# Kernel optimization log

Measured on AMD Instinct MI355X. Metric: run time of the kernel, lower is better.

Reference implementation:

```python
import jax, jax.numpy as jnp
import numpy as np

N = 50000   # nodes
E = 800000  # edges (avg degree 16)
D = 64      # node_feature_dim == node_embedding_dim
L = 4       # num_layers
G = 64      # number of graphs in the batch


def setup_inputs() -> dict:
    key = jax.random.key(0)
    ks = jax.random.split(key, 6)
    x = jax.random.normal(ks[0], (N, D), dtype=jnp.float32)
    edge_index = jax.random.randint(ks[1], (2, E), 0, N, dtype=jnp.int32)
    batch = jnp.sort(jax.random.randint(ks[2], (N,), 0, G, dtype=jnp.int32))
    scale = 1.0 / np.sqrt(D)
    conv_W = jax.random.normal(ks[3], (L, D, D), dtype=jnp.float32) * scale
    conv_b = jnp.zeros((L, D), dtype=jnp.float32)
    lin_W = jax.random.normal(ks[4], (D, 1), dtype=jnp.float32) * scale
    lin_b = jnp.zeros((1,), dtype=jnp.float32)
    return dict(x=x, conv_W=conv_W, conv_b=conv_b, lin_W=lin_W, lin_b=lin_b,
                edge_index=edge_index, batch=batch)


def reference(x, conv_W, conv_b, lin_W, lin_b, edge_index, batch):
    n = x.shape[0]
    # GCNConv: add self-loops, symmetric deg^{-1/2} normalization (computed once; graph is static)
    loop = jnp.arange(n, dtype=edge_index.dtype)
    src = jnp.concatenate([edge_index[0], loop])
    dst = jnp.concatenate([edge_index[1], loop])
    deg = jax.ops.segment_sum(jnp.ones_like(dst, dtype=x.dtype), dst, num_segments=n)
    dinv = jnp.where(deg > 0, jax.lax.rsqrt(deg), 0.0)
    norm = (dinv[src] * dinv[dst])[:, None]  # [E+N, 1]
    # stacked GCNConv + ReLU
    for l in range(conv_W.shape[0]):
        h = x @ conv_W[l]                                       # [N, D] linear transform
        agg = jax.ops.segment_sum(norm * h[src], dst, num_segments=n)  # gather-normalize-scatter
        x = jax.nn.relu(agg + conv_b[l])
    # global_mean_pool over graphs
    counts = jax.ops.segment_sum(jnp.ones((n,), x.dtype), batch, num_segments=G)
    sums = jax.ops.segment_sum(x, batch, num_segments=G)        # [G, D]
    pooled = sums / jnp.maximum(counts, 1.0)[:, None]
    return pooled @ lin_W + lin_b                               # [G, 1]
```

## Files before the change

### kernel.cpp

```cpp
#include <hip/hip_runtime.h>


#define D 64
#define BSHIFT 10
#define BNODES 1024
#define EPT 16
#define CB (256 * EPT)
#define CAP 24576
#define SW(r, c4) ((c4) ^ (((r) >> 2) & 15))


__global__ __launch_bounds__(256) void setup_kernel(
        const float* __restrict__ W, float* __restrict__ Wt,
        int* __restrict__ bcnt, int L) {
    int b = blockIdx.x;
    if (b < L) {
        const float* w = W + (size_t)b * D * D;
        float* wt = Wt + (size_t)b * D * D;
        for (int idx = threadIdx.x; idx < D * D; idx += 256) {
            int k = idx >> 6, c = idx & 63;
            wt[c * D + k] = w[idx];
        }
    } else {
        bcnt[threadIdx.x] = 0;
    }
}


__global__ __launch_bounds__(256) void partition_kernel(
        const int* __restrict__ src, const int* __restrict__ dst,
        int* __restrict__ bcnt, unsigned* __restrict__ eb, int e) {
    __shared__ int cB[256], gb[256], cur[256];
    int t = threadIdx.x;
    cB[t] = 0;
    __syncthreads();
    int base = blockIdx.x * CB;
    int ps[EPT], pd[EPT];
    #pragma unroll
    for (int k = 0; k < EPT; ++k) {
        int i = base + t + k * 256;
        if (i < e) {
            ps[k] = src[i];
            pd[k] = dst[i];
            atomicAdd(&cB[pd[k] >> BSHIFT], 1);
        } else {
            pd[k] = -1;
        }
    }
    __syncthreads();
    if (cB[t]) gb[t] = atomicAdd(&bcnt[t], cB[t]);
    cur[t] = 0;
    __syncthreads();
    #pragma unroll
    for (int k = 0; k < EPT; ++k) {
        if (pd[k] >= 0) {
            int b = pd[k] >> BSHIFT;
            int p = atomicAdd(&cur[b], 1);
            eb[(size_t)b * CAP + gb[b] + p] =
                (unsigned)(ps[k] & 0xFFFF) | ((unsigned)(pd[k] & (BNODES - 1)) << 16);
        }
    }
}

__global__ __launch_bounds__(256) void boff_kernel(
        const int* __restrict__ bcnt, int* __restrict__ boff,
        int* __restrict__ row_start, int n, int e, int nb) {
    __shared__ int sh[256];
    int t = threadIdx.x;
    int c = (t < nb) ? bcnt[t] : 0;
    sh[t] = c;
    __syncthreads();
    for (int off = 1; off < 256; off <<= 1) {
        int vp = (t >= off) ? sh[t - off] : 0;
        __syncthreads();
        sh[t] += vp;
        __syncthreads();
    }
    if (t < nb) boff[t] = sh[t] - c;
    if (t == 255) boff[nb] = sh[255];
    if (t == 0) row_start[n] = e;
}

__global__ __launch_bounds__(BNODES) void build_csr(
        const unsigned* __restrict__ eb, const int* __restrict__ bcnt,
        const int* __restrict__ boff, int* __restrict__ row_start,
        float* __restrict__ dinv, int* __restrict__ csr_src, int n) {
    __shared__ int sh[BNODES];
    __shared__ int cur[BNODES];
    int b = blockIdx.x, t = threadIdx.x;
    int cnt = bcnt[b];
    const unsigned* ebb = eb + (size_t)b * CAP;
    sh[t] = 0;
    __syncthreads();
    for (int i = t; i < cnt; i += BNODES) atomicAdd(&sh[ebb[i] >> 16], 1);
    __syncthreads();
    int c = sh[t];
    __syncthreads();
    for (int off = 1; off < BNODES; off <<= 1) {
        int vp = (t >= off) ? sh[t - off] : 0;
        __syncthreads();
        sh[t] += vp;
        __syncthreads();
    }
    int a = sh[t] - c + boff[b];
    int node = b * BNODES + t;
    if (node < n) {
        row_start[node] = a;
        dinv[node] = 1.0f / sqrtf((float)(c + 1));
    }
    cur[t] = a;
    __syncthreads();
    for (int i = t; i < cnt; i += BNODES) {
        unsigned v = ebb[i];
        int p = atomicAdd(&cur[v >> 16], 1);
        csr_src[p] = (int)(v & 0xFFFFu);
    }
}


__global__ __launch_bounds__(256, 3) void matmul_kernel(
        const float* __restrict__ X, const float* __restrict__ Wt,
        const float* __restrict__ dinv, float* __restrict__ H, int n) {
    __shared__ float4 Xs[64 * 16];
    __shared__ float4 Ws[64 * 16];
    int t = threadIdx.x;
    int rowBase = blockIdx.x * 64;
    const float4* X4 = (const float4*)X;
    const float4* Wt4 = (const float4*)Wt;
    #pragma unroll
    for (int p = 0; p < 4; ++p) {
        int rl = (t >> 4) + 16 * p;
        int c4 = t & 15;
        int r = rowBase + rl;
        float4 v = make_float4(0.f, 0.f, 0.f, 0.f);
        if (r < n) v = X4[(size_t)r * 16 + c4];
        Xs[rl * 16 + SW(rl, c4)] = v;
        Ws[rl * 16 + SW(rl, c4)] = Wt4[rl * 16 + c4];
    }
    __syncthreads();
    int wv = t >> 6, lane = t & 63;
    int rg = lane >> 2, cg = lane & 3;
    int r0 = rg * 4;
    int c0 = wv * 16 + cg * 4;
    float acc[4][4] = {};
    #pragma unroll 2
    for (int k4 = 0; k4 < 16; ++k4) {
        float4 xv[4], wvv[4];
        #pragma unroll
        for (int i = 0; i < 4; ++i) xv[i] = Xs[(r0 + i) * 16 + SW(r0 + i, k4)];
        #pragma unroll
        for (int j = 0; j < 4; ++j) wvv[j] = Ws[(c0 + j) * 16 + SW(c0 + j, k4)];
        #pragma unroll
        for (int i = 0; i < 4; ++i)
            #pragma unroll
            for (int j = 0; j < 4; ++j) {
                acc[i][j] += xv[i].x * wvv[j].x;
                acc[i][j] += xv[i].y * wvv[j].y;
                acc[i][j] += xv[i].z * wvv[j].z;
                acc[i][j] += xv[i].w * wvv[j].w;
            }
    }
    #pragma unroll
    for (int i = 0; i < 4; ++i) {
        int r = rowBase + r0 + i;
        if (r < n) {
            float dr = dinv[r];
            float4 o = make_float4(dr * acc[i][0], dr * acc[i][1],
                                   dr * acc[i][2], dr * acc[i][3]);
            *(float4*)&H[(size_t)r * D + c0] = o;
        }
    }
}


__global__ __launch_bounds__(256) void agg_fused(
        const float* __restrict__ H, const int* __restrict__ csr_src,
        const int* __restrict__ row_start, const float* __restrict__ dinv,
        const float* __restrict__ bias, const float* __restrict__ Wtn,
        float* __restrict__ out, int n) {
    __shared__ float4 Wsh4[D * 16];
    __shared__ float rowsh[4][D];
    int t = threadIdx.x;
    {
        const float4* Wt4 = (const float4*)Wtn;
        #pragma unroll
        for (int p = 0; p < 4; ++p) {
            int i = t + p * 256;
            int c = i >> 4, k4 = i & 15;
            Wsh4[(c << 4) | (k4 ^ (c & 15))] = Wt4[i];
        }
    }
    __syncthreads();
    int wave = t >> 6, lane = t & 63;
    int v = blockIdx.x * 4 + wave;
    bool active = v < n;
    float dv = 0.f, o = 0.f;
    if (active) {
        dv = dinv[v];
        float acc = H[(size_t)v * D + lane];
        int s = row_start[v];
        int e = row_start[v + 1];
        int i = s;
        #pragma unroll 1
        for (; i + 16 <= e; i += 16) {
            int u[16];
            float h[16];
            #pragma unroll
            for (int k = 0; k < 16; ++k) u[k] = csr_src[i + k];
            #pragma unroll
            for (int k = 0; k < 16; ++k) h[k] = H[(size_t)u[k] * D + lane];
            #pragma unroll
            for (int k = 0; k < 16; ++k) acc += h[k];
        }
        #pragma unroll 1
        for (; i + 4 <= e; i += 4) {
            int u0 = csr_src[i + 0], u1 = csr_src[i + 1];
            int u2 = csr_src[i + 2], u3 = csr_src[i + 3];
            float h0 = H[(size_t)u0 * D + lane];
            float h1 = H[(size_t)u1 * D + lane];
            float h2 = H[(size_t)u2 * D + lane];
            float h3 = H[(size_t)u3 * D + lane];
            acc += h0;
            acc += h1;
            acc += h2;
            acc += h3;
        }
        for (; i < e; ++i) {
            int u = csr_src[i];
            acc += H[(size_t)u * D + lane];
        }
        o = fmaxf(dv * acc + bias[lane], 0.f);
    }
    rowsh[wave][lane] = o;
    if (active) {
        const float4* r4p = (const float4*)&rowsh[wave][0];
        float accT = 0.f;
        #pragma unroll
        for (int k4 = 0; k4 < 16; ++k4) {
            float4 r = r4p[k4];
            float4 w = Wsh4[(lane << 4) | (k4 ^ (lane & 15))];
            accT += r.x * w.x;
            accT += r.y * w.y;
            accT += r.z * w.z;
            accT += r.w * w.w;
        }
        out[(size_t)v * D + lane] = dv * accT;
    }
}


__global__ __launch_bounds__(256) void agg_kernel(
        const float* __restrict__ H, const int* __restrict__ csr_src,
        const int* __restrict__ row_start, const float* __restrict__ dinv,
        const float* __restrict__ bias, float* __restrict__ out, int n) {
    int wave = threadIdx.x >> 6, lane = threadIdx.x & 63;
    int v = blockIdx.x * 4 + wave;
    if (v >= n) return;
    float dv = dinv[v];
    float acc = H[(size_t)v * D + lane];
    int s = row_start[v];
    int e = row_start[v + 1];
    int i = s;
    #pragma unroll 1
    for (; i + 16 <= e; i += 16) {
        int u[16];
        float h[16];
        #pragma unroll
        for (int k = 0; k < 16; ++k) u[k] = csr_src[i + k];
        #pragma unroll
        for (int k = 0; k < 16; ++k) h[k] = H[(size_t)u[k] * D + lane];
        #pragma unroll
        for (int k = 0; k < 16; ++k) acc += h[k];
    }
    #pragma unroll 1
    for (; i + 4 <= e; i += 4) {
        int u0 = csr_src[i + 0], u1 = csr_src[i + 1];
        int u2 = csr_src[i + 2], u3 = csr_src[i + 3];
        float h0 = H[(size_t)u0 * D + lane];
        float h1 = H[(size_t)u1 * D + lane];
        float h2 = H[(size_t)u2 * D + lane];
        float h3 = H[(size_t)u3 * D + lane];
        acc += h0;
        acc += h1;
        acc += h2;
        acc += h3;
    }
    for (; i < e; ++i) {
        int u = csr_src[i];
        acc += H[(size_t)u * D + lane];
    }
    out[(size_t)v * D + lane] = fmaxf(dv * acc + bias[lane], 0.f);
}


__device__ __forceinline__ int lower_bound_g(const int* __restrict__ b, int n, int g) {
    int lo = 0, hi = n;
    while (lo < hi) { int m = (lo + hi) >> 1; if (b[m] < g) lo = m + 1; else hi = m; }
    return lo;
}

__global__ __launch_bounds__(1024) void pool_final(
        const float* __restrict__ X, const int* __restrict__ batch,
        const float* __restrict__ linW, const float* __restrict__ linb,
        float* __restrict__ out, int n) {
    __shared__ float sh[16][64];
    int g = blockIdx.x;
    int gs = lower_bound_g(batch, n, g);
    int ge = lower_bound_g(batch, n, g + 1);
    int wv = threadIdx.x >> 6, lane = threadIdx.x & 63;
    float acc = 0.f;
    for (int r = gs + wv; r < ge; r += 16)
        acc += X[(size_t)r * D + lane];
    sh[wv][lane] = acc;
    __syncthreads();
    if (wv == 0) {
        float tot = 0.f;
        #pragma unroll
        for (int i = 0; i < 16; ++i) tot += sh[i][lane];
        float cnt = fmaxf((float)(ge - gs), 1.f);
        float p = (tot / cnt) * linW[lane];
        #pragma unroll
        for (int off = 32; off > 0; off >>= 1) p += __shfl_down(p, off, 64);
        if (lane == 0) out[g] = p + linb[0];
    }
}


extern "C" void kernel_launch(void* const* d_in, const int* in_sizes, int n_in,
                              void* d_out, int out_size, void* d_ws, size_t ws_size,
                              hipStream_t stream) {
    const float* x      = (const float*)d_in[0];
    const float* conv_W = (const float*)d_in[1];
    const float* conv_b = (const float*)d_in[2];
    const float* lin_W  = (const float*)d_in[3];
    const float* lin_b  = (const float*)d_in[4];
    const int*   edge   = (const int*)d_in[5];
    const int*   batch  = (const int*)d_in[6];

    const int n = in_sizes[0] / D;
    const int e = in_sizes[5] / 2;
    const int L = in_sizes[1] / (D * D);
    const int G = out_size;

    const int* esrc = edge;
    const int* edst = edge + e;

    char* ws = (char*)d_ws;
    size_t off = 0;
    auto alloc = [&](size_t bytes) -> void* {
        void* p = ws + off;
        off += (bytes + 255) & ~(size_t)255;
        return p;
    };
    const int nb = (n + BNODES - 1) / BNODES;
    int*   bcnt      = (int*)alloc(256 * 4);
    int*   boff      = (int*)alloc(257 * 4);
    float* dinv      = (float*)alloc((size_t)n * 4);
    int*   row_start = (int*)alloc((size_t)(n + 1) * 4);
    int*   csr_src   = (int*)alloc((size_t)e * 4);
    float* wtbuf     = (float*)alloc((size_t)L * D * D * 4);
    float* hbuf      = (float*)alloc((size_t)n * D * 4);
    float* xbuf      = (float*)alloc((size_t)n * D * 4);
    unsigned* eb     = (unsigned*)hbuf;
    (void)ws_size;

    setup_kernel<<<L + 1, 256, 0, stream>>>(conv_W, wtbuf, bcnt, L);

    const int pb = (e + CB - 1) / CB;
    partition_kernel<<<pb, 256, 0, stream>>>(esrc, edst, bcnt, eb, e);
    boff_kernel     <<<1, 256, 0, stream>>>(bcnt, boff, row_start, n, e, nb);
    build_csr       <<<nb, BNODES, 0, stream>>>(eb, bcnt, boff, row_start, dinv,
                                                csr_src, n);

    const int ablocks = (n + 3) / 4;

    matmul_kernel<<<(n + 63) / 64, 256, 0, stream>>>(x, wtbuf, dinv, hbuf, n);
    agg_fused<<<ablocks, 256, 0, stream>>>(hbuf, csr_src, row_start, dinv,
                                           conv_b + 0 * D, wtbuf + 1 * D * D, xbuf, n);
    agg_fused<<<ablocks, 256, 0, stream>>>(xbuf, csr_src, row_start, dinv,
                                           conv_b + 1 * D, wtbuf + 2 * D * D, hbuf, n);
    agg_fused<<<ablocks, 256, 0, stream>>>(hbuf, csr_src, row_start, dinv,
                                           conv_b + 2 * D, wtbuf + 3 * D * D, xbuf, n);
    agg_kernel<<<ablocks, 256, 0, stream>>>(xbuf, csr_src, row_start, dinv,
                                            conv_b + 3 * D, hbuf, n);

    pool_final<<<G, 1024, 0, stream>>>(hbuf, batch, lin_W, lin_b, (float*)d_out, n);
}
```

Baseline: 227.0 us.

## Store intermediate node features in fp16 and fold block offset scan into CSR build

Intermediate transformed features between layers are now stored as fp16 and converted back to fp32 on load, with accumulation kept in fp32. This halves the bytes moved by the gather-heavy aggregation kernels. Separately, the single-block prefix-scan kernel is removed and each CSR-build block sums the preceding bucket counts itself, saving one launch. The fp16 storage adds rounding error that could affect accuracy tolerance, and the per-lane 2-byte gathers may use memory transactions less efficiently.

Result: faster. 206.1 us, median of 2 (-9.2%).

```diff
diff --git a/kernel.cpp b/kernel.cpp
--- a/kernel.cpp
+++ b/kernel.cpp
@@ -1,4 +1,5 @@
 #include <hip/hip_runtime.h>
+#include <hip/hip_fp16.h>
 
 
 #define D 64
@@ -62,36 +63,22 @@
     }
 }
 
-__global__ __launch_bounds__(256) void boff_kernel(
-        const int* __restrict__ bcnt, int* __restrict__ boff,
-        int* __restrict__ row_start, int n, int e, int nb) {
-    __shared__ int sh[256];
-    int t = threadIdx.x;
-    int c = (t < nb) ? bcnt[t] : 0;
-    sh[t] = c;
-    __syncthreads();
-    for (int off = 1; off < 256; off <<= 1) {
-        int vp = (t >= off) ? sh[t - off] : 0;
-        __syncthreads();
-        sh[t] += vp;
-        __syncthreads();
-    }
-    if (t < nb) boff[t] = sh[t] - c;
-    if (t == 255) boff[nb] = sh[255];
-    if (t == 0) row_start[n] = e;
-}
-
 __global__ __launch_bounds__(BNODES) void build_csr(
         const unsigned* __restrict__ eb, const int* __restrict__ bcnt,
-        const int* __restrict__ boff, int* __restrict__ row_start,
-        float* __restrict__ dinv, int* __restrict__ csr_src, int n) {
+        int* __restrict__ row_start, float* __restrict__ dinv,
+        int* __restrict__ csr_src, int n, int e) {
     __shared__ int sh[BNODES];
     __shared__ int cur[BNODES];
+    __shared__ int boffsh;
     int b = blockIdx.x, t = threadIdx.x;
+    if (t == 0) boffsh = 0;
+    __syncthreads();
+    if (t < b) atomicAdd(&boffsh, bcnt[t]);
     int cnt = bcnt[b];
     const unsigned* ebb = eb + (size_t)b * CAP;
     sh[t] = 0;
     __syncthreads();
+    int boff = boffsh;
     for (int i = t; i < cnt; i += BNODES) atomicAdd(&sh[ebb[i] >> 16], 1);
     __syncthreads();
     int c = sh[t];
@@ -102,12 +89,13 @@
         sh[t] += vp;
         __syncthreads();
     }
-    int a = sh[t] - c + boff[b];
+    int a = sh[t] - c + boff;
     int node = b * BNODES + t;
     if (node < n) {
         row_start[node] = a;
         dinv[node] = 1.0f / sqrtf((float)(c + 1));
     }
+    if (b == 0 && t == 0) row_start[n] = e;
     cur[t] = a;
     __syncthreads();
     for (int i = t; i < cnt; i += BNODES) {
@@ -120,7 +108,7 @@
 
 __global__ __launch_bounds__(256, 3) void matmul_kernel(
         const float* __restrict__ X, const float* __restrict__ Wt,
-        const float* __restrict__ dinv, float* __restrict__ H, int n) {
+        const float* __restrict__ dinv, __half* __restrict__ H, int n) {
     __shared__ float4 Xs[64 * 16];
     __shared__ float4 Ws[64 * 16];
     int t = threadIdx.x;
@@ -165,19 +153,22 @@
         int r = rowBase + r0 + i;
         if (r < n) {
             float dr = dinv[r];
-            float4 o = make_float4(dr * acc[i][0], dr * acc[i][1],
-                                   dr * acc[i][2], dr * acc[i][3]);
-            *(float4*)&H[(size_t)r * D + c0] = o;
+            ushort4 o;
+            o.x = __half_as_ushort(__float2half(dr * acc[i][0]));
+            o.y = __half_as_ushort(__float2half(dr * acc[i][1]));
+            o.z = __half_as_ushort(__float2half(dr * acc[i][2]));
+            o.w = __half_as_ushort(__float2half(dr * acc[i][3]));
+            *(ushort4*)&H[(size_t)r * D + c0] = o;
         }
     }
 }
 
 
 __global__ __launch_bounds__(256) void agg_fused(
-        const float* __restrict__ H, const int* __restrict__ csr_src,
+        const __half* __restrict__ H, const int* __restrict__ csr_src,
         const int* __restrict__ row_start, const float* __restrict__ dinv,
         const float* __restrict__ bias, const float* __restrict__ Wtn,
-        float* __restrict__ out, int n) {
+        __half* __restrict__ out, int n) {
     __shared__ float4 Wsh4[D * 16];
     __shared__ float rowsh[4][D];
     int t = threadIdx.x;
@@ -197,7 +188,7 @@
     float dv = 0.f, o = 0.f;
     if (active) {
         dv = dinv[v];
-        float acc = H[(size_t)v * D + lane];
+        float acc = __half2float(H[(size_t)v * D + lane]);
         int s = row_start[v];
         int e = row_start[v + 1];
         int i = s;
@@ -208,7 +199,7 @@
             #pragma unroll
             for (int k = 0; k < 16; ++k) u[k] = csr_src[i + k];
             #pragma unroll
-            for (int k = 0; k < 16; ++k) h[k] = H[(size_t)u[k] * D + lane];
+            for (int k = 0; k < 16; ++k) h[k] = __half2float(H[(size_t)u[k] * D + lane]);
             #pragma unroll
             for (int k = 0; k < 16; ++k) acc += h[k];
         }
@@ -216,10 +207,10 @@
         for (; i + 4 <= e; i += 4) {
             int u0 = csr_src[i + 0], u1 = csr_src[i + 1];
             int u2 = csr_src[i + 2], u3 = csr_src[i + 3];
-            float h0 = H[(size_t)u0 * D + lane];
-            float h1 = H[(size_t)u1 * D + lane];
-            float h2 = H[(size_t)u2 * D + lane];
-            float h3 = H[(size_t)u3 * D + lane];
+            float h0 = __half2float(H[(size_t)u0 * D + lane]);
+            float h1 = __half2float(H[(size_t)u1 * D + lane]);
+            float h2 = __half2float(H[(size_t)u2 * D + lane]);
+            float h3 = __half2float(H[(size_t)u3 * D + lane]);
             acc += h0;
             acc += h1;
             acc += h2;
@@ -227,7 +218,7 @@
         }
         for (; i < e; ++i) {
             int u = csr_src[i];
-            acc += H[(size_t)u * D + lane];
+            acc += __half2float(H[(size_t)u * D + lane]);
         }
         o = fmaxf(dv * acc + bias[lane], 0.f);
     }
@@ -244,20 +235,20 @@
             accT += r.z * w.z;
             accT += r.w * w.w;
         }
-        out[(size_t)v * D + lane] = dv * accT;
+        out[(size_t)v * D + lane] = __float2half(dv * accT);
     }
 }
 
 
 __global__ __launch_bounds__(256) void agg_kernel(
-        const float* __restrict__ H, const int* __restrict__ csr_src,
+        const __half* __restrict__ H, const int* __restrict__ csr_src,
         const int* __restrict__ row_start, const float* __restrict__ dinv,
         const float* __restrict__ bias, float* __restrict__ out, int n) {
     int wave = threadIdx.x >> 6, lane = threadIdx.x & 63;
     int v = blockIdx.x * 4 + wave;
     if (v >= n) return;
     float dv = dinv[v];
-    float acc = H[(size_t)v * D + lane];
+    float acc = __half2float(H[(size_t)v * D + lane]);
     int s = row_start[v];
     int e = row_start[v + 1];
     int i = s;
@@ -268,7 +259,7 @@
         #pragma unroll
         for (int k = 0; k < 16; ++k) u[k] = csr_src[i + k];
         #pragma unroll
-        for (int k = 0; k < 16; ++k) h[k] = H[(size_t)u[k] * D + lane];
+        for (int k = 0; k < 16; ++k) h[k] = __half2float(H[(size_t)u[k] * D + lane]);
         #pragma unroll
         for (int k = 0; k < 16; ++k) acc += h[k];
     }
@@ -276,10 +267,10 @@
     for (; i + 4 <= e; i += 4) {
         int u0 = csr_src[i + 0], u1 = csr_src[i + 1];
         int u2 = csr_src[i + 2], u3 = csr_src[i + 3];
-        float h0 = H[(size_t)u0 * D + lane];
-        float h1 = H[(size_t)u1 * D + lane];
-        float h2 = H[(size_t)u2 * D + lane];
-        float h3 = H[(size_t)u3 * D + lane];
+        float h0 = __half2float(H[(size_t)u0 * D + lane]);
+        float h1 = __half2float(H[(size_t)u1 * D + lane]);
+        float h2 = __half2float(H[(size_t)u2 * D + lane]);
+        float h3 = __half2float(H[(size_t)u3 * D + lane]);
         acc += h0;
         acc += h1;
         acc += h2;
@@ -287,7 +278,7 @@
     }
     for (; i < e; ++i) {
         int u = csr_src[i];
-        acc += H[(size_t)u * D + lane];
+        acc += __half2float(H[(size_t)u * D + lane]);
     }
     out[(size_t)v * D + lane] = fmaxf(dv * acc + bias[lane], 0.f);
 }
@@ -353,36 +344,35 @@
         return p;
     };
     const int nb = (n + BNODES - 1) / BNODES;
-    int*   bcnt      = (int*)alloc(256 * 4);
-    int*   boff      = (int*)alloc(257 * 4);
-    float* dinv      = (float*)alloc((size_t)n * 4);
-    int*   row_start = (int*)alloc((size_t)(n + 1) * 4);
-    int*   csr_src   = (int*)alloc((size_t)e * 4);
-    float* wtbuf     = (float*)alloc((size_t)L * D * D * 4);
-    float* hbuf      = (float*)alloc((size_t)n * D * 4);
-    float* xbuf      = (float*)alloc((size_t)n * D * 4);
-    unsigned* eb     = (unsigned*)hbuf;
+    int*    bcnt      = (int*)alloc(256 * 4);
+    float*  dinv      = (float*)alloc((size_t)n * 4);
+    int*    row_start = (int*)alloc((size_t)(n + 1) * 4);
+    int*    csr_src   = (int*)alloc((size_t)e * 4);
+    float*  wtbuf     = (float*)alloc((size_t)L * D * D * 4);
+    __half* h16a      = (__half*)alloc((size_t)n * D * 2);
+    __half* h16b      = (__half*)alloc((size_t)n * D * 2);
+    float*  hf32      = (float*)alloc((size_t)n * D * 4);
+    unsigned* eb      = (unsigned*)hf32;
     (void)ws_size;
 
     setup_kernel<<<L + 1, 256, 0, stream>>>(conv_W, wtbuf, bcnt, L);
 
     const int pb = (e + CB - 1) / CB;
     partition_kernel<<<pb, 256, 0, stream>>>(esrc, edst, bcnt, eb, e);
-    boff_kernel     <<<1, 256, 0, stream>>>(bcnt, boff, row_start, n, e, nb);
-    build_csr       <<<nb, BNODES, 0, stream>>>(eb, bcnt, boff, row_start, dinv,
-                                                csr_src, n);
+    build_csr       <<<nb, BNODES, 0, stream>>>(eb, bcnt, row_start, dinv,
+                                                csr_src, n, e);
 
     const int ablocks = (n + 3) / 4;
 
-    matmul_kernel<<<(n + 63) / 64, 256, 0, stream>>>(x, wtbuf, dinv, hbuf, n);
-    agg_fused<<<ablocks, 256, 0, stream>>>(hbuf, csr_src, row_start, dinv,
-                                           conv_b + 0 * D, wtbuf + 1 * D * D, xbuf, n);
-    agg_fused<<<ablocks, 256, 0, stream>>>(xbuf, csr_src, row_start, dinv,
-                                           conv_b + 1 * D, wtbuf + 2 * D * D, hbuf, n);
-    agg_fused<<<ablocks, 256, 0, stream>>>(hbuf, csr_src, row_start, dinv,
-                                           conv_b + 2 * D, wtbuf + 3 * D * D, xbuf, n);
-    agg_kernel<<<ablocks, 256, 0, stream>>>(xbuf, csr_src, row_start, dinv,
-                                            conv_b + 3 * D, hbuf, n);
-
-    pool_final<<<G, 1024, 0, stream>>>(hbuf, batch, lin_W, lin_b, (float*)d_out, n);
-}
+    matmul_kernel<<<(n + 63) / 64, 256, 0, stream>>>(x, wtbuf, dinv, h16a, n);
+    agg_fused<<<ablocks, 256, 0, stream>>>(h16a, csr_src, row_start, dinv,
+                                           conv_b + 0 * D, wtbuf + 1 * D * D, h16b, n);
+    agg_fused<<<ablocks, 256, 0, stream>>>(h16b, csr_src, row_start, dinv,
+                                           conv_b + 1 * D, wtbuf + 2 * D * D, h16a, n);
+    agg_fused<<<ablocks, 256, 0, stream>>>(h16a, csr_src, row_start, dinv,
+                                           conv_b + 2 * D, wtbuf + 3 * D * D, h16b, n);
+    agg_kernel<<<ablocks, 256, 0, stream>>>(h16b, csr_src, row_start, dinv,
+                                            conv_b + 3 * D, hf32, n);
+
+    pool_final<<<G, 1024, 0, stream>>>(hf32, batch, lin_W, lin_b, (float*)d_out, n);
+}
```
